# Kernel optimization log

Measured on AMD Instinct MI355X. Metric: run time of the kernel, lower is better.

Reference implementation:

```python
import jax, jax.numpy as jnp
import numpy as np

B, C, T = 8, 128, 8192
SIGMA_MIN = 1e-6

def setup_inputs() -> dict:
    key = jax.random.key(0)
    ks = jax.random.split(key, 9)
    x1 = jax.random.normal(ks[0], (B, C, T), dtype=jnp.float32)
    mu = jax.random.normal(ks[1], (B, C, T), dtype=jnp.float32)
    style = jax.random.normal(ks[2], (B, 192), dtype=jnp.float32)
    t_sample = jax.random.uniform(ks[3], (B, 1, 1), dtype=jnp.float32)
    z = jax.random.normal(ks[4], (B, C, T), dtype=jnp.float32)
    W = jax.random.normal(ks[5], (C, C), dtype=jnp.float32) * (1.0 / np.sqrt(C))
    b_lin = jax.random.normal(ks[6], (C,), dtype=jnp.float32) * 0.01
    prompt_lens = jax.random.randint(ks[7], (B,), 64, T // 4)
    x_lens = jax.random.randint(ks[8], (B,), T // 2, T)
    return {"x1": x1, "mu": mu, "style": style, "t_sample": t_sample, "z": z,
            "W": W, "b_lin": b_lin, "x_lens": x_lens, "prompt_lens": prompt_lens}

def reference(x1, mu, style, t_sample, z, W, b_lin, x_lens, prompt_lens):
    # x1, z: [B, C, T]; t_sample: [B, 1, 1]
    sigma = SIGMA_MIN
    Bb, Cc, Tt = x1.shape
    tpos = jnp.arange(Tt)
    pmask = tpos[None, :] < prompt_lens[:, None]            # [B, T] prompt region
    # flow-matching interpolation
    y = (1.0 - (1.0 - sigma) * t_sample) * z + t_sample * x1
    u = x1 - (1.0 - sigma) * z
    # zero out prompt region of y (prompt copy tensor is unused by the mock estimator)
    y = jnp.where(pmask[:, None, :], 0.0, y)
    # mock estimator: per-timestep Linear over channels
    out = jnp.einsum('bct,dc->bdt', y, W) + b_lin[None, :, None]
    # per-sample MSE over [prompt_lens, x_lens) across all channels, then mean over batch
    lmask = (~pmask) & (tpos[None, :] < x_lens[:, None])     # [B, T]
    diff2 = jnp.square(out - u) * lmask[:, None, :]
    counts = (Cc * jnp.sum(lmask, axis=1)).astype(x1.dtype)  # [B]
    loss = jnp.mean(jnp.sum(diff2, axis=(1, 2)) / counts)
    return loss, out + (1.0 - sigma) * z
```

## Files before the change

kernel.cpp:

```cpp
#include <hip/hip_runtime.h>
#include <hip/hip_bf16.h>

#define BB   8
#define CC   128
#define TLEN 8192
#define TBLK 128
#define NB   (BB * (TLEN / TBLK))
#define WS_W_OFF 8192

typedef __attribute__((ext_vector_type(8))) short short8;
typedef __attribute__((ext_vector_type(4))) float f32x4;

__device__ __forceinline__ short f2bf(float f) {
    union { float f; unsigned u; } v; v.f = f;
    return (short)((v.u + 0x7FFFu + ((v.u >> 16) & 1u)) >> 16);
}
__device__ __forceinline__ float bf2f(unsigned short h) {
    union { unsigned u; float f; } v; v.u = ((unsigned)h) << 16;
    return v.f;
}
__device__ __forceinline__ int swz(int t, int c) {
    return c ^ (((t ^ (t >> 3)) & 15) << 3);
}

__global__ void prep_w(const float* __restrict__ W, short* __restrict__ wsW) {
    const int gid   = blockIdx.x * 256 + threadIdx.x;
    const int lane  = gid & 63;
    const int ksdt  = gid >> 6;
    const int dtile = ksdt >> 2;
    const int ks    = ksdt & 3;
    const int row   = dtile * 16 + (lane & 15);
    const int col0  = ks * 32 + (lane >> 4) * 8;
    short8 a;
    #pragma unroll
    for (int e = 0; e < 8; ++e) a[e] = f2bf(W[row * CC + col0 + e]);
    reinterpret_cast<short8*>(wsW)[gid] = a;
}

__global__ __launch_bounds__(512, 4)
void cfm_main(const float* __restrict__ x1, const float* __restrict__ tsm,
              const float* __restrict__ z, const short* __restrict__ wsW,
              const float* __restrict__ blin, const int* __restrict__ xlens,
              const int* __restrict__ plens, float* __restrict__ out,
              float* __restrict__ wsPart)
{
    __shared__ short xt[TBLK][CC];
    __shared__ short zt[TBLK][CC];
    __shared__ float red[8];

    const int bi = blockIdx.x;
    const int b  = bi & 7;
    const int t0 = (bi >> 3) * TBLK;

    const int tid  = threadIdx.x;
    const int lane = tid & 63;
    const int wid  = tid >> 6;
    const int r15  = lane & 15;
    const int q4   = lane >> 4;

    const float ts  = tsm[b];
    const int   pl  = plens[b];
    const int   xl  = xlens[b];
    const float oms = 0.999999f;
    const float cz  = 1.0f - oms * ts;
    const float cx  = ts;

    const int tpart = (tid & 31) * 4;
    const int c0    = tid >> 5;
    const size_t rowb = (size_t)b * CC * TLEN + (size_t)t0 + tpart;

    float4 xv[8], zv[8];
    #pragma unroll
    for (int p = 0; p < 8; ++p)
        xv[p] = *reinterpret_cast<const float4*>(x1 + rowb + (size_t)(c0 + p * 16) * TLEN);
    #pragma unroll
    for (int p = 0; p < 8; ++p)
        zv[p] = *reinterpret_cast<const float4*>(z + rowb + (size_t)(c0 + p * 16) * TLEN);

    short8 af[4];
    {
        const short8* wf = reinterpret_cast<const short8*>(wsW);
        #pragma unroll
        for (int ks = 0; ks < 4; ++ks)
            af[ks] = wf[(wid * 4 + ks) * 64 + lane];
    }

    #pragma unroll
    for (int p = 0; p < 8; ++p) {
        const int c = c0 + p * 16;
        const float* xs = reinterpret_cast<const float*>(&xv[p]);
        const float* zs = reinterpret_cast<const float*>(&zv[p]);
        #pragma unroll
        for (int j = 0; j < 4; ++j) {
            const int t  = tpart + j;
            const int cs = swz(t, c);
            xt[t][cs] = f2bf(xs[j]);
            zt[t][cs] = f2bf(zs[j]);
        }
    }
    __syncthreads();

    f32x4 aX[8], aZ[8];
    #pragma unroll
    for (int tt = 0; tt < 8; ++tt) { aX[tt] = (f32x4){0,0,0,0}; aZ[tt] = (f32x4){0,0,0,0}; }

    #pragma unroll
    for (int ks = 0; ks < 4; ++ks) {
        #pragma unroll
        for (int tt = 0; tt < 8; ++tt) {
            const int tr = tt * 16 + r15;
            const int cs = swz(tr, ks * 32 + q4 * 8);
            const short8 xa = *reinterpret_cast<const short8*>(&xt[tr][cs]);
            const short8 za = *reinterpret_cast<const short8*>(&zt[tr][cs]);
            aX[tt] = __builtin_amdgcn_mfma_f32_16x16x32_bf16(af[ks], xa, aX[tt], 0, 0, 0);
            aZ[tt] = __builtin_amdgcn_mfma_f32_16x16x32_bf16(af[ks], za, aZ[tt], 0, 0, 0);
        }
    }

    float lsum = 0.0f;
    #pragma unroll
    for (int rr = 0; rr < 4; ++rr) {
        const int d  = wid * 16 + q4 * 4 + rr;
        const float bl = blin[d];
        float* orow = out + 1 + (size_t)(b * CC + d) * TLEN + t0;
        #pragma unroll
        for (int tt = 0; tt < 8; ++tt) {
            const int tl = tt * 16 + r15;
            const int tg = t0 + tl;
            const float s  = cx * aX[tt][rr] + cz * aZ[tt][rr];
            const bool pm  = tg >= pl;
            const float ov = (pm ? s : 0.0f) + bl;
            const int cs   = swz(tl, d);
            const float w  = oms * bf2f((unsigned short)zt[tl][cs]);
            orow[tl] = ov + w;
            if (pm & (tg < xl)) {
                const float xf = bf2f((unsigned short)xt[tl][cs]);
                const float df = ov - (xf - w);
                lsum += df * df;
            }
        }
    }

    #pragma unroll
    for (int off = 32; off >= 1; off >>= 1) lsum += __shfl_down(lsum, off);
    if (lane == 0) red[wid] = lsum;
    __syncthreads();
    if (tid == 0) {
        const float scale = 1.0f / (1024.0f * (float)(xl - pl));
        float s = 0.0f;
        #pragma unroll
        for (int w = 0; w < 8; ++w) s += red[w];
        wsPart[bi] = s * scale;
    }
}

__global__ void final_red(const float* __restrict__ wsPart, float* __restrict__ out) {
    __shared__ float red[4];
    const int tid = threadIdx.x;
    float s = 0.0f;
    #pragma unroll
    for (int i = 0; i < NB / 256; ++i) s += wsPart[tid + i * 256];
    #pragma unroll
    for (int off = 32; off >= 1; off >>= 1) s += __shfl_down(s, off);
    if ((tid & 63) == 0) red[tid >> 6] = s;
    __syncthreads();
    if (tid == 0) out[0] = red[0] + red[1] + red[2] + red[3];
}

extern "C" void kernel_launch(void* const* d_in, const int* in_sizes, int n_in,
                              void* d_out, int out_size, void* d_ws, size_t ws_size,
                              hipStream_t stream) {
    const float* x1    = (const float*)d_in[0];
    const float* tsm   = (const float*)d_in[3];
    const float* z     = (const float*)d_in[4];
    const float* W     = (const float*)d_in[5];
    const float* blin  = (const float*)d_in[6];
    const int*   xlens = (const int*)d_in[7];
    const int*   plens = (const int*)d_in[8];
    float* out = (float*)d_out;

    float* wsPart = (float*)d_ws;
    short* wsW    = (short*)((char*)d_ws + WS_W_OFF);

    prep_w<<<8, 256, 0, stream>>>(W, wsW);
    cfm_main<<<NB, 512, 0, stream>>>(x1, tsm, z, wsW, blin, xlens, plens, out, wsPart);
    final_red<<<1, 256, 0, stream>>>(wsPart, out);
}
```

Before: 31.09 us.

## Fuse weight prep and final reduction into main kernel, split tile into two halves

Each block now converts W to bf16 fragments itself and accumulates the loss with an atomicAdd, so the separate prep and final-reduction kernels are gone and a memset replaces them. The 128-timestep tile is processed as two 64-step halves, with the second half's global loads issued before the first half's compute to overlap them. This removes two launches and halves the register footprint for accumulators, at the cost of redundant W conversion per block and atomic contention on one float.

New measurement: 53.83 us. 73.1% more time.

```diff
diff --git a/kernel.cpp b/kernel.cpp
--- a/kernel.cpp
+++ b/kernel.cpp
@@ -4,9 +4,9 @@
 #define BB   8
 #define CC   128
 #define TLEN 8192
+#define TT   64
 #define TBLK 128
 #define NB   (BB * (TLEN / TBLK))
-#define WS_W_OFF 8192
 
 typedef __attribute__((ext_vector_type(8))) short short8;
 typedef __attribute__((ext_vector_type(4))) float f32x4;
@@ -23,29 +23,61 @@
     return c ^ (((t ^ (t >> 3)) & 15) << 3);
 }
 
-__global__ void prep_w(const float* __restrict__ W, short* __restrict__ wsW) {
-    const int gid   = blockIdx.x * 256 + threadIdx.x;
-    const int lane  = gid & 63;
-    const int ksdt  = gid >> 6;
-    const int dtile = ksdt >> 2;
-    const int ks    = ksdt & 3;
-    const int row   = dtile * 16 + (lane & 15);
-    const int col0  = ks * 32 + (lane >> 4) * 8;
-    short8 a;
+__device__ __forceinline__ void compute_tile(
+    const short (*xb)[CC], const short (*zb)[CC], const short8 (&af)[4],
+    int wid, int r15, int q4, int tbase, int b, int pl, int xl,
+    float cx, float cz, float oms, const float* __restrict__ blin,
+    float* __restrict__ out, float& lsum)
+{
+    f32x4 aX[4], aZ[4];
     #pragma unroll
-    for (int e = 0; e < 8; ++e) a[e] = f2bf(W[row * CC + col0 + e]);
-    reinterpret_cast<short8*>(wsW)[gid] = a;
+    for (int tt = 0; tt < 4; ++tt) { aX[tt] = (f32x4){0,0,0,0}; aZ[tt] = (f32x4){0,0,0,0}; }
+
+    #pragma unroll
+    for (int ks = 0; ks < 4; ++ks) {
+        #pragma unroll
+        for (int tt = 0; tt < 4; ++tt) {
+            const int tr = tt * 16 + r15;
+            const int cs = swz(tr, ks * 32 + q4 * 8);
+            const short8 xa = *reinterpret_cast<const short8*>(&xb[tr][cs]);
+            const short8 za = *reinterpret_cast<const short8*>(&zb[tr][cs]);
+            aX[tt] = __builtin_amdgcn_mfma_f32_16x16x32_bf16(af[ks], xa, aX[tt], 0, 0, 0);
+            aZ[tt] = __builtin_amdgcn_mfma_f32_16x16x32_bf16(af[ks], za, aZ[tt], 0, 0, 0);
+        }
+    }
+
+    #pragma unroll
+    for (int rr = 0; rr < 4; ++rr) {
+        const int d  = wid * 16 + q4 * 4 + rr;
+        const float bl = blin[d];
+        float* orow = out + 1 + (size_t)(b * CC + d) * TLEN + tbase;
+        #pragma unroll
+        for (int tt = 0; tt < 4; ++tt) {
+            const int tl = tt * 16 + r15;
+            const int tg = tbase + tl;
+            const float s  = cx * aX[tt][rr] + cz * aZ[tt][rr];
+            const bool pm  = tg >= pl;
+            const float ov = (pm ? s : 0.0f) + bl;
+            const int cs   = swz(tl, d);
+            const float w  = oms * bf2f((unsigned short)zb[tl][cs]);
+            orow[tl] = ov + w;
+            if (pm & (tg < xl)) {
+                const float xf = bf2f((unsigned short)xb[tl][cs]);
+                const float df = ov - (xf - w);
+                lsum += df * df;
+            }
+        }
+    }
 }
 
 __global__ __launch_bounds__(512, 4)
-void cfm_main(const float* __restrict__ x1, const float* __restrict__ tsm,
-              const float* __restrict__ z, const short* __restrict__ wsW,
-              const float* __restrict__ blin, const int* __restrict__ xlens,
-              const int* __restrict__ plens, float* __restrict__ out,
-              float* __restrict__ wsPart)
+void cfm_fused(const float* __restrict__ x1, const float* __restrict__ tsm,
+               const float* __restrict__ z, const float* __restrict__ W,
+               const float* __restrict__ blin, const int* __restrict__ xlens,
+               const int* __restrict__ plens, float* __restrict__ out)
 {
-    __shared__ short xt[TBLK][CC];
-    __shared__ short zt[TBLK][CC];
+    __shared__ short xt[2][TT][CC];
+    __shared__ short zt[2][TT][CC];
     __shared__ float red[8];
 
     const int bi = blockIdx.x;
@@ -65,106 +97,82 @@
     const float cz  = 1.0f - oms * ts;
     const float cx  = ts;
 
-    const int tpart = (tid & 31) * 4;
-    const int c0    = tid >> 5;
-    const size_t rowb = (size_t)b * CC * TLEN + (size_t)t0 + tpart;
+    const int tj = (tid & 15) * 4;
+    const int cr = tid >> 4;
+    const size_t gb0 = (size_t)b * CC * TLEN + (size_t)t0 + tj;
 
-    float4 xv[8], zv[8];
+    float4 xv[4], zv[4];
     #pragma unroll
-    for (int p = 0; p < 8; ++p)
-        xv[p] = *reinterpret_cast<const float4*>(x1 + rowb + (size_t)(c0 + p * 16) * TLEN);
-    #pragma unroll
-    for (int p = 0; p < 8; ++p)
-        zv[p] = *reinterpret_cast<const float4*>(z + rowb + (size_t)(c0 + p * 16) * TLEN);
+    for (int p = 0; p < 4; ++p) {
+        xv[p] = *reinterpret_cast<const float4*>(x1 + gb0 + (size_t)(cr + p * 32) * TLEN);
+        zv[p] = *reinterpret_cast<const float4*>(z  + gb0 + (size_t)(cr + p * 32) * TLEN);
+    }
 
     short8 af[4];
     {
-        const short8* wf = reinterpret_cast<const short8*>(wsW);
+        const int row = wid * 16 + r15;
         #pragma unroll
-        for (int ks = 0; ks < 4; ++ks)
-            af[ks] = wf[(wid * 4 + ks) * 64 + lane];
+        for (int ks = 0; ks < 4; ++ks) {
+            const float4 w0 = *reinterpret_cast<const float4*>(W + row * CC + ks * 32 + q4 * 8);
+            const float4 w1 = *reinterpret_cast<const float4*>(W + row * CC + ks * 32 + q4 * 8 + 4);
+            short8 a;
+            a[0] = f2bf(w0.x); a[1] = f2bf(w0.y); a[2] = f2bf(w0.z); a[3] = f2bf(w0.w);
+            a[4] = f2bf(w1.x); a[5] = f2bf(w1.y); a[6] = f2bf(w1.z); a[7] = f2bf(w1.w);
+            af[ks] = a;
+        }
     }
 
     #pragma unroll
-    for (int p = 0; p < 8; ++p) {
-        const int c = c0 + p * 16;
+    for (int p = 0; p < 4; ++p) {
+        const int c = cr + p * 32;
         const float* xs = reinterpret_cast<const float*>(&xv[p]);
         const float* zs = reinterpret_cast<const float*>(&zv[p]);
         #pragma unroll
         for (int j = 0; j < 4; ++j) {
-            const int t  = tpart + j;
+            const int t  = tj + j;
             const int cs = swz(t, c);
-            xt[t][cs] = f2bf(xs[j]);
-            zt[t][cs] = f2bf(zs[j]);
+            xt[0][t][cs] = f2bf(xs[j]);
+            zt[0][t][cs] = f2bf(zs[j]);
+        }
+    }
+
+    #pragma unroll
+    for (int p = 0; p < 4; ++p) {
+        xv[p] = *reinterpret_cast<const float4*>(x1 + gb0 + TT + (size_t)(cr + p * 32) * TLEN);
+        zv[p] = *reinterpret_cast<const float4*>(z  + gb0 + TT + (size_t)(cr + p * 32) * TLEN);
+    }
+    __syncthreads();
+
+    float lsum = 0.0f;
+    compute_tile(xt[0], zt[0], af, wid, r15, q4, t0, b, pl, xl, cx, cz, oms, blin, out, lsum);
+
+    #pragma unroll
+    for (int p = 0; p < 4; ++p) {
+        const int c = cr + p * 32;
+        const float* xs = reinterpret_cast<const float*>(&xv[p]);
+        const float* zs = reinterpret_cast<const float*>(&zv[p]);
+        #pragma unroll
+        for (int j = 0; j < 4; ++j) {
+            const int t  = tj + j;
+            const int cs = swz(t, c);
+            xt[1][t][cs] = f2bf(xs[j]);
+            zt[1][t][cs] = f2bf(zs[j]);
         }
     }
     __syncthreads();
 
-    f32x4 aX[8], aZ[8];
-    #pragma unroll
-    for (int tt = 0; tt < 8; ++tt) { aX[tt] = (f32x4){0,0,0,0}; aZ[tt] = (f32x4){0,0,0,0}; }
-
-    #pragma unroll
-    for (int ks = 0; ks < 4; ++ks) {
-        #pragma unroll
-        for (int tt = 0; tt < 8; ++tt) {
-            const int tr = tt * 16 + r15;
-            const int cs = swz(tr, ks * 32 + q4 * 8);
-            const short8 xa = *reinterpret_cast<const short8*>(&xt[tr][cs]);
-            const short8 za = *reinterpret_cast<const short8*>(&zt[tr][cs]);
-            aX[tt] = __builtin_amdgcn_mfma_f32_16x16x32_bf16(af[ks], xa, aX[tt], 0, 0, 0);
-            aZ[tt] = __builtin_amdgcn_mfma_f32_16x16x32_bf16(af[ks], za, aZ[tt], 0, 0, 0);
-        }
-    }
-
-    float lsum = 0.0f;
-    #pragma unroll
-    for (int rr = 0; rr < 4; ++rr) {
-        const int d  = wid * 16 + q4 * 4 + rr;
-        const float bl = blin[d];
-        float* orow = out + 1 + (size_t)(b * CC + d) * TLEN + t0;
-        #pragma unroll
-        for (int tt = 0; tt < 8; ++tt) {
-            const int tl = tt * 16 + r15;
-            const int tg = t0 + tl;
-            const float s  = cx * aX[tt][rr] + cz * aZ[tt][rr];
-            const bool pm  = tg >= pl;
-            const float ov = (pm ? s : 0.0f) + bl;
-            const int cs   = swz(tl, d);
-            const float w  = oms * bf2f((unsigned short)zt[tl][cs]);
-            orow[tl] = ov + w;
-            if (pm & (tg < xl)) {
-                const float xf = bf2f((unsigned short)xt[tl][cs]);
-                const float df = ov - (xf - w);
-                lsum += df * df;
-            }
-        }
-    }
+    compute_tile(xt[1], zt[1], af, wid, r15, q4, t0 + TT, b, pl, xl, cx, cz, oms, blin, out, lsum);
 
     #pragma unroll
     for (int off = 32; off >= 1; off >>= 1) lsum += __shfl_down(lsum, off);
     if (lane == 0) red[wid] = lsum;
     __syncthreads();
     if (tid == 0) {
-        const float scale = 1.0f / (1024.0f * (float)(xl - pl));
         float s = 0.0f;
         #pragma unroll
         for (int w = 0; w < 8; ++w) s += red[w];
-        wsPart[bi] = s * scale;
+        atomicAdd(out, s / (1024.0f * (float)(xl - pl)));
     }
-}
-
-__global__ void final_red(const float* __restrict__ wsPart, float* __restrict__ out) {
-    __shared__ float red[4];
-    const int tid = threadIdx.x;
-    float s = 0.0f;
-    #pragma unroll
-    for (int i = 0; i < NB / 256; ++i) s += wsPart[tid + i * 256];
-    #pragma unroll
-    for (int off = 32; off >= 1; off >>= 1) s += __shfl_down(s, off);
-    if ((tid & 63) == 0) red[tid >> 6] = s;
-    __syncthreads();
-    if (tid == 0) out[0] = red[0] + red[1] + red[2] + red[3];
 }
 
 extern "C" void kernel_launch(void* const* d_in, const int* in_sizes, int n_in,
@@ -179,10 +187,6 @@
     const int*   plens = (const int*)d_in[8];
     float* out = (float*)d_out;
 
-    float* wsPart = (float*)d_ws;
-    short* wsW    = (short*)((char*)d_ws + WS_W_OFF);
-
-    prep_w<<<8, 256, 0, stream>>>(W, wsW);
-    cfm_main<<<NB, 512, 0, stream>>>(x1, tsm, z, wsW, blin, xlens, plens, out, wsPart);
-    final_red<<<1, 256, 0, stream>>>(wsPart, out);
+    hipMemsetAsync(out, 0, sizeof(float), stream);
+    cfm_fused<<<NB, 512, 0, stream>>>(x1, tsm, z, W, blin, xlens, plens, out);
 }
```

## Fuse weight conversion and final loss reduction into the main kernel

Applied to the files above, without the earlier changes.

Drops the separate weight-prep kernel: each wave now loads its fp32 W fragment directly and converts it to bf16 in registers. Drops the single-block final reduction kernel: each block atomically adds its scaled partial loss into the output, which a memset zeroes beforehand. This removes two kernel launches and the workspace round trips. In exchange, every block re-reads and re-converts W, and the loss sum order becomes nondeterministic.

After: 32.40 us. 1.04x slower.

```diff
diff --git a/kernel.cpp b/kernel.cpp
--- a/kernel.cpp
+++ b/kernel.cpp
@@ -6,7 +6,6 @@
 #define TLEN 8192
 #define TBLK 128
 #define NB   (BB * (TLEN / TBLK))
-#define WS_W_OFF 8192
 
 typedef __attribute__((ext_vector_type(8))) short short8;
 typedef __attribute__((ext_vector_type(4))) float f32x4;
@@ -23,26 +22,11 @@
     return c ^ (((t ^ (t >> 3)) & 15) << 3);
 }
 
-__global__ void prep_w(const float* __restrict__ W, short* __restrict__ wsW) {
-    const int gid   = blockIdx.x * 256 + threadIdx.x;
-    const int lane  = gid & 63;
-    const int ksdt  = gid >> 6;
-    const int dtile = ksdt >> 2;
-    const int ks    = ksdt & 3;
-    const int row   = dtile * 16 + (lane & 15);
-    const int col0  = ks * 32 + (lane >> 4) * 8;
-    short8 a;
-    #pragma unroll
-    for (int e = 0; e < 8; ++e) a[e] = f2bf(W[row * CC + col0 + e]);
-    reinterpret_cast<short8*>(wsW)[gid] = a;
-}
-
 __global__ __launch_bounds__(512, 4)
-void cfm_main(const float* __restrict__ x1, const float* __restrict__ tsm,
-              const float* __restrict__ z, const short* __restrict__ wsW,
-              const float* __restrict__ blin, const int* __restrict__ xlens,
-              const int* __restrict__ plens, float* __restrict__ out,
-              float* __restrict__ wsPart)
+void cfm_fused(const float* __restrict__ x1, const float* __restrict__ tsm,
+               const float* __restrict__ z, const float* __restrict__ W,
+               const float* __restrict__ blin, const int* __restrict__ xlens,
+               const int* __restrict__ plens, float* __restrict__ out)
 {
     __shared__ short xt[TBLK][CC];
     __shared__ short zt[TBLK][CC];
@@ -79,10 +63,16 @@
 
     short8 af[4];
     {
-        const short8* wf = reinterpret_cast<const short8*>(wsW);
+        const int row = wid * 16 + r15;
         #pragma unroll
-        for (int ks = 0; ks < 4; ++ks)
-            af[ks] = wf[(wid * 4 + ks) * 64 + lane];
+        for (int ks = 0; ks < 4; ++ks) {
+            const float4 w0 = *reinterpret_cast<const float4*>(W + row * CC + ks * 32 + q4 * 8);
+            const float4 w1 = *reinterpret_cast<const float4*>(W + row * CC + ks * 32 + q4 * 8 + 4);
+            short8 a;
+            a[0] = f2bf(w0.x); a[1] = f2bf(w0.y); a[2] = f2bf(w0.z); a[3] = f2bf(w0.w);
+            a[4] = f2bf(w1.x); a[5] = f2bf(w1.y); a[6] = f2bf(w1.z); a[7] = f2bf(w1.w);
+            af[ks] = a;
+        }
     }
 
     #pragma unroll
@@ -146,25 +136,11 @@
     if (lane == 0) red[wid] = lsum;
     __syncthreads();
     if (tid == 0) {
-        const float scale = 1.0f / (1024.0f * (float)(xl - pl));
         float s = 0.0f;
         #pragma unroll
         for (int w = 0; w < 8; ++w) s += red[w];
-        wsPart[bi] = s * scale;
+        atomicAdd(out, s / (1024.0f * (float)(xl - pl)));
     }
-}
-
-__global__ void final_red(const float* __restrict__ wsPart, float* __restrict__ out) {
-    __shared__ float red[4];
-    const int tid = threadIdx.x;
-    float s = 0.0f;
-    #pragma unroll
-    for (int i = 0; i < NB / 256; ++i) s += wsPart[tid + i * 256];
-    #pragma unroll
-    for (int off = 32; off >= 1; off >>= 1) s += __shfl_down(s, off);
-    if ((tid & 63) == 0) red[tid >> 6] = s;
-    __syncthreads();
-    if (tid == 0) out[0] = red[0] + red[1] + red[2] + red[3];
 }
 
 extern "C" void kernel_launch(void* const* d_in, const int* in_sizes, int n_in,
@@ -179,10 +155,6 @@
     const int*   plens = (const int*)d_in[8];
     float* out = (float*)d_out;
 
-    float* wsPart = (float*)d_ws;
-    short* wsW    = (short*)((char*)d_ws + WS_W_OFF);
-
-    prep_w<<<8, 256, 0, stream>>>(W, wsW);
-    cfm_main<<<NB, 512, 0, stream>>>(x1, tsm, z, wsW, blin, xlens, plens, out, wsPart);
-    final_red<<<1, 256, 0, stream>>>(wsPart, out);
+    hipMemsetAsync(out, 0, sizeof(float), stream);
+    cfm_fused<<<NB, 512, 0, stream>>>(x1, tsm, z, W, blin, xlens, plens, out);
 }
```
